# Kernel optimization log

Measured on AMD Instinct MI355X. Metric: run time of the kernel, lower is better.

## Reference

```python
import jax, jax.numpy as jnp
import numpy as np

MAX_FRAMES = 12
EMBED_DIM = 512
TOPK = 12
NUM_SAMPLES = 500
SIGMA = 0.05
SEL_DIM = 2
NUM_HEADS = 2


def setup_inputs() -> dict:
    key = jax.random.key(0)
    ks = jax.random.split(key, 9)
    D = EMBED_DIM
    C = D // 2
    s = lambda fan_in: 1.0 / np.sqrt(fan_in)
    return {
        "x": jax.random.normal(ks[0], (16, MAX_FRAMES * 50, D), dtype=jnp.float32),
        "ln_g": jnp.ones((D,), jnp.float32),
        "ln_b": jnp.zeros((D,), jnp.float32),
        "w_in": jax.random.normal(ks[1], (D, C), jnp.float32) * s(D),
        "wq": jax.random.normal(ks[2], (C, C), jnp.float32) * s(C),
        "wk": jax.random.normal(ks[3], (C, C), jnp.float32) * s(C),
        "wv": jax.random.normal(ks[4], (C, C), jnp.float32) * s(C),
        "wo": jax.random.normal(ks[5], (C, C), jnp.float32) * s(C),
        "w1": jax.random.normal(ks[6], (2 * C, C), jnp.float32) * s(2 * C),
        "w2": jax.random.normal(ks[7], (C, 1), jnp.float32) * s(C),
    }


def layer_norm(x, g, b, eps=1e-5):
    mu = jnp.mean(x, axis=-1, keepdims=True)
    var = jnp.var(x, axis=-1, keepdims=True)
    return (x - mu) * jax.lax.rsqrt(var + eps) * g + b


def mha(x, wq, wk, wv, wo):
    B, N, C = x.shape
    hd = C // NUM_HEADS
    q = (x @ wq).reshape(B, N, NUM_HEADS, hd).transpose(0, 2, 1, 3)
    k = (x @ wk).reshape(B, N, NUM_HEADS, hd).transpose(0, 2, 1, 3)
    v = (x @ wv).reshape(B, N, NUM_HEADS, hd).transpose(0, 2, 1, 3)
    attn = jax.nn.softmax(jnp.einsum('bhnd,bhmd->bhnm', q, k) / np.sqrt(hd), axis=-1)
    out = jnp.einsum('bhnm,bhmd->bhnd', attn, v).transpose(0, 2, 1, 3).reshape(B, N, C)
    return out @ wo


def predictor(x, ln_g, ln_b, w_in, wq, wk, wv, wo, w1, w2):
    h = jax.nn.gelu(layer_norm(x, ln_g, ln_b) @ w_in, approximate=False)
    h = mha(h, wq, wk, wv, wo)
    B, N, C = h.shape
    g = jnp.mean(h, axis=1, keepdims=True)
    h = jnp.concatenate([h, jnp.broadcast_to(g, (B, N, C))], axis=-1)
    h = jax.nn.gelu(h @ w1, approximate=False)
    return jnp.tanh(h @ w2)  # (B, N, 1)


def perturbed_topk(scores):
    # scores: (b, d) -> soft indicators (b, k, d)
    b, d = scores.shape
    noise = jax.random.normal(jax.random.key(1), (b, NUM_SAMPLES, d), dtype=scores.dtype)
    perturbed = scores[:, None, :] + noise * SIGMA
    _, idx = jax.lax.top_k(perturbed, TOPK)            # (b, ns, k)
    idx = jnp.sort(idx, axis=-1)
    onehot = jax.nn.one_hot(idx, d, dtype=scores.dtype)  # (b, ns, k, d)
    return onehot.mean(axis=1)                          # (b, k, d)


def reference(x, ln_g, ln_b, w_in, wq, wk, wv, wo, w1, w2):
    B, L, D = x.shape
    N = L // MAX_FRAMES
    xf = x.reshape(B * MAX_FRAMES, N, D)
    pred = predictor(xf, ln_g, ln_b, w_in, wq, wk, wv, wo, w1, w2)[..., 0]  # (b, N)
    spatial_score = pred[:, SEL_DIM:]                    # (b, N-2)
    ind = perturbed_topk(spatial_score)                  # (b, k, N-2)
    cls_feat = xf[:, :SEL_DIM, :]
    spatial_feat = xf[:, SEL_DIM:, :]
    sel = jnp.einsum('bkl,bld->bkd', ind, spatial_feat)
    out = jnp.concatenate([cls_feat, sel], axis=1)       # (b, 2+k, D)
    return out.reshape(B, -1, D)
```

## Files before the change

kernel.cpp:

```cpp
#include <hip/hip_runtime.h>
#include <stdint.h>

#define B2      192
#define NTOK    50
#define ROWS    9600
#define D_EMB   512
#define C_DIM   256
#define HD      128
#define NSAMP   500
#define TOPKK   12
#define NSPA    48

typedef short short8 __attribute__((ext_vector_type(8)));
typedef float f32x4  __attribute__((ext_vector_type(4)));

__device__ __forceinline__ float gelu_f(float x) {
    return 0.5f * x * (1.0f + erff(x * 0.7071067811865476f));
}
__device__ __forceinline__ uint16_t f2bf(float x) {
    uint32_t u = __float_as_uint(x);
    return (uint16_t)((u + 0x7fffu + ((u >> 16) & 1u)) >> 16);
}
__device__ __forceinline__ float bf2f(uint16_t b) {
    return __uint_as_float(((uint32_t)b) << 16);
}
__device__ __forceinline__ size_t swzA(int m, int k, int K) {
    return ((size_t)(m >> 4) * (K >> 5) + (k >> 5)) * 512
         + (size_t)((((k >> 3) & 3) * 16 + (m & 15)) * 8 + (k & 7));
}

__global__ __launch_bounds__(256) void prep_kernel(const float* __restrict__ x,
                                                   const float* __restrict__ g,
                                                   const float* __restrict__ b,
                                                   short* __restrict__ xh,
                                                   short* __restrict__ xl,
                                                   const float* __restrict__ w_in, const float* __restrict__ wq,
                                                   const float* __restrict__ wk, const float* __restrict__ wv,
                                                   const float* __restrict__ wo, const float* __restrict__ w1,
                                                   short* win_hi, short* win_lo, short* wq_hi, short* wq_lo,
                                                   short* wk_hi, short* wk_lo, short* wv_hi, short* wv_lo,
                                                   short* wo_hi, short* wo_lo, short* w1a_hi, short* w1a_lo,
                                                   short* w1b_hi, short* w1b_lo) {
    if (blockIdx.x < 2400) {
        int row  = blockIdx.x * 4 + (threadIdx.x >> 6);
        int lane = threadIdx.x & 63;
        const float* rp = x + (size_t)row * D_EMB;
        float4 v0 = *(const float4*)(rp + lane * 8);
        float4 v1 = *(const float4*)(rp + lane * 8 + 4);
        float s  = v0.x + v0.y + v0.z + v0.w + v1.x + v1.y + v1.z + v1.w;
        float s2 = v0.x*v0.x + v0.y*v0.y + v0.z*v0.z + v0.w*v0.w
                 + v1.x*v1.x + v1.y*v1.y + v1.z*v1.z + v1.w*v1.w;
#pragma unroll
        for (int off = 32; off; off >>= 1) {
            s  += __shfl_xor(s,  off);
            s2 += __shfl_xor(s2, off);
        }
        float mu  = s / 512.0f;
        float var = s2 / 512.0f - mu * mu;
        float inv = 1.0f / sqrtf(var + 1e-5f);
        const float* gp = g + lane * 8;
        const float* bp = b + lane * 8;
        float o[8];
        o[0]=(v0.x-mu)*inv*gp[0]+bp[0]; o[1]=(v0.y-mu)*inv*gp[1]+bp[1];
        o[2]=(v0.z-mu)*inv*gp[2]+bp[2]; o[3]=(v0.w-mu)*inv*gp[3]+bp[3];
        o[4]=(v1.x-mu)*inv*gp[4]+bp[4]; o[5]=(v1.y-mu)*inv*gp[5]+bp[5];
        o[6]=(v1.z-mu)*inv*gp[6]+bp[6]; o[7]=(v1.w-mu)*inv*gp[7]+bp[7];
        short8 h8, l8;
#pragma unroll
        for (int j = 0; j < 8; ++j) {
            uint16_t h = f2bf(o[j]);
            h8[j] = (short)h;
            l8[j] = (short)f2bf(o[j] - bf2f(h));
        }
        size_t blk = (size_t)(row >> 4) * 16 + (lane >> 2);
        int inner  = (lane & 3) * 16 + (row & 15);
        ((short8*)xh)[blk * 64 + inner] = h8;
        ((short8*)xl)[blk * 64 + inner] = l8;
    } else {
        int blk = blockIdx.x - 2400;
        const float* W; short *hi, *lo; int K, base;
        if      (blk <  64) { W = w_in;            hi = win_hi; lo = win_lo; K = 512; base = 0;   }
        else if (blk <  96) { W = wq;              hi = wq_hi;  lo = wq_lo;  K = 256; base = 64;  }
        else if (blk < 128) { W = wk;              hi = wk_hi;  lo = wk_lo;  K = 256; base = 96;  }
        else if (blk < 160) { W = wv;              hi = wv_hi;  lo = wv_lo;  K = 256; base = 128; }
        else if (blk < 192) { W = wo;              hi = wo_hi;  lo = wo_lo;  K = 256; base = 160; }
        else if (blk < 224) { W = w1;              hi = w1a_hi; lo = w1a_lo; K = 256; base = 192; }
        else                { W = w1 + 256 * 256;  hi = w1b_hi; lo = w1b_lo; K = 256; base = 224; }
        int t = (blk - base) * 256 + threadIdx.x;
        int n = t & 255, k8 = t >> 8;
        short8 h8, l8;
#pragma unroll
        for (int j = 0; j < 8; ++j) {
            float wvl = W[(size_t)(k8 * 8 + j) * 256 + n];
            uint16_t h = f2bf(wvl);
            h8[j] = (short)h;
            l8[j] = (short)f2bf(wvl - bf2f(h));
        }
        size_t bb = (size_t)(n >> 4) * (K >> 5) + (k8 >> 2);
        int inner = (k8 & 3) * 16 + (n & 15);
        ((short8*)hi)[bb * 64 + inner] = h8;
        ((short8*)lo)[bb * 64 + inner] = l8;
    }
}

template<int KB>
__device__ __forceinline__ void mm_core(const short8* __restrict__ pAh, const short8* __restrict__ pAl,
                                        const short8* __restrict__ pBh0, const short8* __restrict__ pBl0,
                                        const short8* __restrict__ pBh1, const short8* __restrict__ pBl1,
                                        f32x4& acc0, f32x4& acc1) {
    short8 ah[3], al[3], bh0[3], bl0[3], bh1[3], bl1[3];
#pragma unroll
    for (int i = 0; i < 2; ++i) {
        int off = i * 64;
        ah[i] = pAh[off];  al[i] = pAl[off];
        bh0[i] = pBh0[off]; bl0[i] = pBl0[off];
        bh1[i] = pBh1[off]; bl1[i] = pBl1[off];
    }
#pragma unroll
    for (int ks = 0; ks < KB; ++ks) {
        int cur = ks % 3;
        if (ks + 2 < KB) {
            int pre = (ks + 2) % 3, off = (ks + 2) * 64;
            ah[pre] = pAh[off];  al[pre] = pAl[off];
            bh0[pre] = pBh0[off]; bl0[pre] = pBl0[off];
            bh1[pre] = pBh1[off]; bl1[pre] = pBl1[off];
        }
        acc0 = __builtin_amdgcn_mfma_f32_16x16x32_bf16(ah[cur], bh0[cur], acc0, 0, 0, 0);
        acc0 = __builtin_amdgcn_mfma_f32_16x16x32_bf16(ah[cur], bl0[cur], acc0, 0, 0, 0);
        acc0 = __builtin_amdgcn_mfma_f32_16x16x32_bf16(al[cur], bh0[cur], acc0, 0, 0, 0);
        acc1 = __builtin_amdgcn_mfma_f32_16x16x32_bf16(ah[cur], bh1[cur], acc1, 0, 0, 0);
        acc1 = __builtin_amdgcn_mfma_f32_16x16x32_bf16(ah[cur], bl1[cur], acc1, 0, 0, 0);
        acc1 = __builtin_amdgcn_mfma_f32_16x16x32_bf16(al[cur], bh1[cur], acc1, 0, 0, 0);
    }
}

__device__ __forceinline__ void epi_store(f32x4 acc, int row0, int col, int N,
                                          float* __restrict__ Cf, short* __restrict__ Chi,
                                          short* __restrict__ Clo,
                                          const float* __restrict__ bias, int act) {
#pragma unroll
    for (int r = 0; r < 4; ++r) {
        int row = row0 + r;
        float v2 = acc[r];
        if (bias) v2 += bias[(size_t)(row / 50) * N + col];
        if (act)  v2 = gelu_f(v2);
        if (Cf) Cf[(size_t)row * N + col] = v2;
        if (Chi) {
            uint16_t h = f2bf(v2);
            size_t ad = swzA(row, col, 256);
            Chi[ad] = (short)h;
            Clo[ad] = (short)f2bf(v2 - bf2f(h));
        }
    }
}

template<int KB>
__global__ __launch_bounds__(256) void gemm_one(const short8* __restrict__ Ah,
                                                const short8* __restrict__ Al,
                                                const short8* __restrict__ Bh,
                                                const short8* __restrict__ Bl,
                                                float* __restrict__ Cf,
                                                short* __restrict__ Chi,
                                                short* __restrict__ Clo,
                                                const float* __restrict__ bias,
                                                int act) {
    int lane = threadIdx.x & 63;
    int wv   = threadIdx.x >> 6;
    int ms   = blockIdx.x * 4 + wv;
    int ns0  = blockIdx.y * 2;
    const short8* pAh  = Ah + (size_t)ms  * KB * 64 + lane;
    const short8* pAl  = Al + (size_t)ms  * KB * 64 + lane;
    const short8* pBh0 = Bh + (size_t)ns0 * KB * 64 + lane;
    const short8* pBl0 = Bl + (size_t)ns0 * KB * 64 + lane;
    const short8* pBh1 = pBh0 + (size_t)KB * 64;
    const short8* pBl1 = pBl0 + (size_t)KB * 64;
    f32x4 acc0 = {0.f,0.f,0.f,0.f}, acc1 = {0.f,0.f,0.f,0.f};
    mm_core<KB>(pAh, pAl, pBh0, pBl0, pBh1, pBl1, acc0, acc1);
    int row0 = ms * 16 + (lane >> 4) * 4;
    int cin  = lane & 15;
    epi_store(acc0, row0, ns0 * 16 + cin,      256, Cf, Chi, Clo, bias, act);
    epi_store(acc1, row0, (ns0 + 1) * 16 + cin, 256, Cf, Chi, Clo, bias, act);
}

__global__ __launch_bounds__(256) void gemm_qkv(const short8* __restrict__ Ah,
                                                const short8* __restrict__ Al,
                                                const short8* __restrict__ Bhq, const short8* __restrict__ Blq,
                                                const short8* __restrict__ Bhk, const short8* __restrict__ Blk,
                                                const short8* __restrict__ Bhv, const short8* __restrict__ Blv,
                                                float* __restrict__ q, float* __restrict__ k,
                                                float* __restrict__ v) {
    int lane = threadIdx.x & 63;
    int wv   = threadIdx.x >> 6;
    int ms   = blockIdx.x * 4 + wv;
    int sel  = blockIdx.y >> 3;
    int ns0  = (blockIdx.y & 7) * 2;
    const short8* Bh = (sel == 0) ? Bhq : (sel == 1) ? Bhk : Bhv;
    const short8* Bl = (sel == 0) ? Blq : (sel == 1) ? Blk : Blv;
    float* C = (sel == 0) ? q : (sel == 1) ? k : v;
    const short8* pAh  = Ah + (size_t)ms  * 8 * 64 + lane;
    const short8* pAl  = Al + (size_t)ms  * 8 * 64 + lane;
    const short8* pBh0 = Bh + (size_t)ns0 * 8 * 64 + lane;
    const short8* pBl0 = Bl + (size_t)ns0 * 8 * 64 + lane;
    const short8* pBh1 = pBh0 + 8 * 64;
    const short8* pBl1 = pBl0 + 8 * 64;
    f32x4 acc0 = {0.f,0.f,0.f,0.f}, acc1 = {0.f,0.f,0.f,0.f};
    mm_core<8>(pAh, pAl, pBh0, pBl0, pBh1, pBl1, acc0, acc1);
    int row0 = ms * 16 + (lane >> 4) * 4;
    int cin  = lane & 15;
    epi_store(acc0, row0, ns0 * 16 + cin,      256, C, nullptr, nullptr, nullptr, 0);
    epi_store(acc1, row0, (ns0 + 1) * 16 + cin, 256, C, nullptr, nullptr, nullptr, 0);
}

__global__ __launch_bounds__(256) void attn_kernel(const float* __restrict__ q,
                                                   const float* __restrict__ k,
                                                   const float* __restrict__ v,
                                                   short* __restrict__ aoh,
                                                   short* __restrict__ aol) {
    __shared__ float sQ[NTOK * 132];
    __shared__ float sK[NTOK * 132];
    __shared__ float sS[NTOK * 51];
    int blk = blockIdx.x;
    int b = blk >> 1, h = blk & 1;
    const size_t base = (size_t)b * NTOK * C_DIM + h * HD;
    int tid = threadIdx.x;
    for (int idx = tid; idx < 1600; idx += 256) {
        int r = idx >> 5, c = (idx & 31) * 4;
        *(float4*)&sQ[r * 132 + c] = *(const float4*)(q + base + (size_t)r * C_DIM + c);
        *(float4*)&sK[r * 132 + c] = *(const float4*)(k + base + (size_t)r * C_DIM + c);
    }
    __syncthreads();
    for (int e = tid; e < 625; e += 256) {
        int i2 = e / 25, j2 = e - i2 * 25;
        int i = i2 * 2, j = j2 * 2;
        const float* qi0 = &sQ[i * 132];
        const float* qi1 = qi0 + 132;
        const float* kj0 = &sK[j * 132];
        const float* kj1 = kj0 + 132;
        float4 a00 = {0,0,0,0}, a01 = {0,0,0,0}, a10 = {0,0,0,0}, a11 = {0,0,0,0};
#pragma unroll
        for (int t = 0; t < 32; ++t) {
            float4 q0 = *(const float4*)&qi0[t * 4];
            float4 q1 = *(const float4*)&qi1[t * 4];
            float4 b0 = *(const float4*)&kj0[t * 4];
            float4 b1 = *(const float4*)&kj1[t * 4];
            a00.x = fmaf(q0.x, b0.x, a00.x); a00.y = fmaf(q0.y, b0.y, a00.y);
            a00.z = fmaf(q0.z, b0.z, a00.z); a00.w = fmaf(q0.w, b0.w, a00.w);
            a01.x = fmaf(q0.x, b1.x, a01.x); a01.y = fmaf(q0.y, b1.y, a01.y);
            a01.z = fmaf(q0.z, b1.z, a01.z); a01.w = fmaf(q0.w, b1.w, a01.w);
            a10.x = fmaf(q1.x, b0.x, a10.x); a10.y = fmaf(q1.y, b0.y, a10.y);
            a10.z = fmaf(q1.z, b0.z, a10.z); a10.w = fmaf(q1.w, b0.w, a10.w);
            a11.x = fmaf(q1.x, b1.x, a11.x); a11.y = fmaf(q1.y, b1.y, a11.y);
            a11.z = fmaf(q1.z, b1.z, a11.z); a11.w = fmaf(q1.w, b1.w, a11.w);
        }
        const float sc = 0.08838834764831845f;
        sS[i * 51 + j]           = (a00.x + a00.y + a00.z + a00.w) * sc;
        sS[i * 51 + j + 1]       = (a01.x + a01.y + a01.z + a01.w) * sc;
        sS[(i + 1) * 51 + j]     = (a10.x + a10.y + a10.z + a10.w) * sc;
        sS[(i + 1) * 51 + j + 1] = (a11.x + a11.y + a11.z + a11.w) * sc;
    }
    __syncthreads();
    for (int idx = tid; idx < 1600; idx += 256) {
        int r = idx >> 5, c = (idx & 31) * 4;
        *(float4*)&sQ[r * 132 + c] = *(const float4*)(v + base + (size_t)r * C_DIM + c);
    }
    if (tid < NTOK) {
        float* row = &sS[tid * 51];
        float m = row[0];
        for (int j = 1; j < NTOK; ++j) m = fmaxf(m, row[j]);
        float sum = 0.f;
        for (int j = 0; j < NTOK; ++j) { float e2 = expf(row[j] - m); row[j] = e2; sum += e2; }
        float inv = 1.0f / sum;
        for (int j = 0; j < NTOK; ++j) row[j] *= inv;
    }
    __syncthreads();
    for (int e = tid; e < 1600; e += 256) {
        int i = e >> 5, d4 = (e & 31) * 4;
        const float* srow = &sS[i * 51];
        float4 acc = {0,0,0,0};
#pragma unroll
        for (int j = 0; j < NTOK; ++j) {
            float w = srow[j];
            float4 v4 = *(const float4*)&sQ[j * 132 + d4];
            acc.x = fmaf(w, v4.x, acc.x); acc.y = fmaf(w, v4.y, acc.y);
            acc.z = fmaf(w, v4.z, acc.z); acc.w = fmaf(w, v4.w, acc.w);
        }
        int row = b * NTOK + i;
        float vals[4] = {acc.x, acc.y, acc.z, acc.w};
#pragma unroll
        for (int c = 0; c < 4; ++c) {
            int col = h * HD + d4 + c;
            uint16_t hh = f2bf(vals[c]);
            size_t ad = swzA(row, col, 256);
            aoh[ad] = (short)hh;
            aol[ad] = (short)f2bf(vals[c] - bf2f(hh));
        }
    }
}

__global__ __launch_bounds__(256) void mean50(const float* __restrict__ h2,
                                              short* __restrict__ gh,
                                              short* __restrict__ gl) {
    int b = blockIdx.x, c = threadIdx.x;
    float s = 0.f;
    for (int n = 0; n < NTOK; ++n) s += h2[((size_t)b * NTOK + n) * C_DIM + c];
    float g = s / 50.0f;
    uint16_t h = f2bf(g);
    size_t ad = swzA(b, c, 256);
    gh[ad] = (short)h;
    gl[ad] = (short)f2bf(g - bf2f(h));
}

__global__ __launch_bounds__(256) void matvec_tanh(const float* __restrict__ h3,
                                                   const float* __restrict__ w2,
                                                   float* __restrict__ pred) {
    int row  = blockIdx.x * 4 + (threadIdx.x >> 6);
    int lane = threadIdx.x & 63;
    const float* rp = h3 + (size_t)row * C_DIM;
    float4 a = *(const float4*)(rp + lane * 4);
    float4 w = *(const float4*)(w2 + lane * 4);
    float s = a.x * w.x + a.y * w.y + a.z * w.z + a.w * w.w;
#pragma unroll
    for (int off = 32; off; off >>= 1) s += __shfl_xor(s, off);
    if (lane == 0) pred[row] = tanhf(s);
}

__device__ __forceinline__ uint32_t rotl32(uint32_t x, int r) {
    return (x << r) | (x >> (32 - r));
}
__device__ __forceinline__ void threefry01(uint32_t& x0, uint32_t& x1) {
    const uint32_t ks0 = 0u, ks1 = 1u, ks2 = 0x1BD11BDBu;
    x0 += ks0; x1 += ks1;
#define TFR(r) { x0 += x1; x1 = rotl32(x1, r); x1 ^= x0; }
    TFR(13) TFR(15) TFR(26) TFR(6)  x0 += ks1; x1 += ks2 + 1u;
    TFR(17) TFR(29) TFR(16) TFR(24) x0 += ks2; x1 += ks0 + 2u;
    TFR(13) TFR(15) TFR(26) TFR(6)  x0 += ks0; x1 += ks1 + 3u;
    TFR(17) TFR(29) TFR(16) TFR(24) x0 += ks1; x1 += ks2 + 4u;
    TFR(13) TFR(15) TFR(26) TFR(6)  x0 += ks2; x1 += ks0 + 5u;
#undef TFR
}

__device__ __forceinline__ float erfinv_xla(float x) {
    float w = -log1pf(-x * x);
    float p;
    if (w < 5.0f) {
        w -= 2.5f;
        p = 2.81022636e-08f;
        p = fmaf(p, w, 3.43273939e-07f);
        p = fmaf(p, w, -3.5233877e-06f);
        p = fmaf(p, w, -4.39150654e-06f);
        p = fmaf(p, w, 0.00021858087f);
        p = fmaf(p, w, -0.00125372503f);
        p = fmaf(p, w, -0.00417768164f);
        p = fmaf(p, w, 0.246640727f);
        p = fmaf(p, w, 1.50140941f);
    } else {
        w = sqrtf(w) - 3.0f;
        p = -0.000200214257f;
        p = fmaf(p, w, 0.000100950558f);
        p = fmaf(p, w, 0.00134934322f);
        p = fmaf(p, w, -0.00367342844f);
        p = fmaf(p, w, 0.00573950773f);
        p = fmaf(p, w, -0.0076224613f);
        p = fmaf(p, w, 0.00943887047f);
        p = fmaf(p, w, 1.00167406f);
        p = fmaf(p, w, 2.83297682f);
    }
    return p * x;
}

__device__ __forceinline__ float bits_to_normal(uint32_t bits) {
    float f = __uint_as_float((bits >> 9) | 0x3f800000u) - 1.0f;
    float u = f * 2.0f + (-0.99999994039535522461f);
    u = fmaxf(-0.99999994039535522461f, u);
    return 1.4142135623730951f * erfinv_xla(u);
}

__device__ __forceinline__ unsigned long long topk_key(uint32_t base, int d,
                                                       const float* __restrict__ sp) {
    uint32_t x0 = 0u, x1 = base + (uint32_t)d;
    threefry01(x0, x1);
    float n  = bits_to_normal(x0 ^ x1);
    float v  = sp[d] + n * 0.05f;
    uint32_t vb   = __float_as_uint(v);
    uint32_t mono = (vb & 0x80000000u) ? ~vb : (vb | 0x80000000u);
    return ((unsigned long long)mono << 6) | (unsigned)(63 - d);
}

__global__ __launch_bounds__(256, 4) void topk_kernel(const float* __restrict__ pred,
                                                      int* __restrict__ counts) {
    __shared__ unsigned long long sK[128][13];
    int lane = threadIdx.x & 63;
    int wv   = threadIdx.x >> 6;
    int p    = wv >> 1;
    int hh   = wv & 1;
    int g    = blockIdx.x * 128 + p * 64 + lane;
    int b    = g / NSAMP;
    int s    = g - b * NSAMP;
    uint32_t base = (uint32_t)((b * NSAMP + s) * NSPA);
    const float* sp = pred + b * NTOK + 2;
    int d0 = hh * 24;

    unsigned long long l0=0ull,l1=0ull,l2=0ull,l3=0ull,l4=0ull,l5=0ull,
                       l6=0ull,l7=0ull,l8=0ull,l9=0ull,l10=0ull,l11=0ull;
    unsigned long long key;

#define STEP(li) { unsigned long long mn_ = (key < li) ? key : li; \
                   li = (key > li) ? key : li; key = mn_; }
#define S1  STEP(l0)
#define S2  S1  STEP(l1)
#define S3  S2  STEP(l2)
#define S4  S3  STEP(l3)
#define S5  S4  STEP(l4)
#define S6  S5  STEP(l5)
#define S7  S6  STEP(l6)
#define S8  S7  STEP(l7)
#define S9  S8  STEP(l8)
#define S10 S9  STEP(l9)
#define S11 S10 STEP(l10)
#define S12 S11 STEP(l11)

    key = topk_key(base, d0 + 0,  sp); S1
    key = topk_key(base, d0 + 1,  sp); S2
    key = topk_key(base, d0 + 2,  sp); S3
    key = topk_key(base, d0 + 3,  sp); S4
    key = topk_key(base, d0 + 4,  sp); S5
    key = topk_key(base, d0 + 5,  sp); S6
    key = topk_key(base, d0 + 6,  sp); S7
    key = topk_key(base, d0 + 7,  sp); S8
    key = topk_key(base, d0 + 8,  sp); S9
    key = topk_key(base, d0 + 9,  sp); S10
    key = topk_key(base, d0 + 10, sp); S11
    key = topk_key(base, d0 + 11, sp); S12
#pragma unroll 2
    for (int dd = 12; dd < 24; ++dd) {
        key = topk_key(base, d0 + dd, sp); S12
    }

    int rowL = p * 64 + lane;
    if (hh == 1) {
        unsigned long long* r = sK[rowL];
        r[0]=l0; r[1]=l1; r[2]=l2;  r[3]=l3;  r[4]=l4;   r[5]=l5;
        r[6]=l6; r[7]=l7; r[8]=l8;  r[9]=l9;  r[10]=l10; r[11]=l11;
    }
    __syncthreads();
    if (hh == 0) {
        const unsigned long long* r = sK[rowL];
        unsigned long long M0  = (l0  > r[11]) ? l0  : r[11];
        unsigned long long M1  = (l1  > r[10]) ? l1  : r[10];
        unsigned long long M2  = (l2  > r[9])  ? l2  : r[9];
        unsigned long long M3  = (l3  > r[8])  ? l3  : r[8];
        unsigned long long M4  = (l4  > r[7])  ? l4  : r[7];
        unsigned long long M5  = (l5  > r[6])  ? l5  : r[6];
        unsigned long long M6  = (l6  > r[5])  ? l6  : r[5];
        unsigned long long M7  = (l7  > r[4])  ? l7  : r[4];
        unsigned long long M8  = (l8  > r[3])  ? l8  : r[3];
        unsigned long long M9  = (l9  > r[2])  ? l9  : r[2];
        unsigned long long M10 = (l10 > r[1])  ? l10 : r[1];
        unsigned long long M11 = (l11 > r[0])  ? l11 : r[0];
        unsigned long long m = 0ull;
        m |= 1ull << (unsigned)(M0  & 63ull);  m |= 1ull << (unsigned)(M1  & 63ull);
        m |= 1ull << (unsigned)(M2  & 63ull);  m |= 1ull << (unsigned)(M3  & 63ull);
        m |= 1ull << (unsigned)(M4  & 63ull);  m |= 1ull << (unsigned)(M5  & 63ull);
        m |= 1ull << (unsigned)(M6  & 63ull);  m |= 1ull << (unsigned)(M7  & 63ull);
        m |= 1ull << (unsigned)(M8  & 63ull);  m |= 1ull << (unsigned)(M9  & 63ull);
        m |= 1ull << (unsigned)(M10 & 63ull);  m |= 1ull << (unsigned)(M11 & 63ull);
#define EMIT(Mi) { unsigned a_ = (unsigned)(Mi & 63ull); \
                   int kpos_ = 11 - __popcll(m & ((1ull << a_) - 1ull)); \
                   int d_ = 63 - (int)a_; \
                   atomicAdd(&counts[((size_t)b * TOPKK + kpos_) * NSPA + d_], 1); }
        EMIT(M0)  EMIT(M1)  EMIT(M2)  EMIT(M3)  EMIT(M4)  EMIT(M5)
        EMIT(M6)  EMIT(M7)  EMIT(M8)  EMIT(M9)  EMIT(M10) EMIT(M11)
#undef EMIT
    }
#undef STEP
#undef S1
#undef S2
#undef S3
#undef S4
#undef S5
#undef S6
#undef S7
#undef S8
#undef S9
#undef S10
#undef S11
#undef S12
}

__global__ __launch_bounds__(256) void select_out(const float* __restrict__ x,
                                                  const int* __restrict__ counts,
                                                  float* __restrict__ out) {
    int row = blockIdx.x;
    int b = row / 14, k = row - b * 14;
    int d = threadIdx.x;
    if (k < 2) {
        out[(size_t)row * D_EMB + d]       = x[((size_t)(b * NTOK + k)) * D_EMB + d];
        out[(size_t)row * D_EMB + d + 256] = x[((size_t)(b * NTOK + k)) * D_EMB + d + 256];
    } else {
        int kk = k - 2;
        const int* cnt = counts + ((size_t)b * TOPKK + kk) * NSPA;
        __shared__ int sc[NSPA];
        if (d < NSPA) sc[d] = cnt[d];
        __syncthreads();
        float a0 = 0.f, a1 = 0.f;
        for (int l = 0; l < NSPA; ++l) {
            int c = sc[l];
            if (c) {
                float w = (float)c / 500.0f;
                const float* xr = x + ((size_t)(b * NTOK + 2 + l)) * D_EMB;
                a0 = fmaf(w, xr[d], a0);
                a1 = fmaf(w, xr[d + 256], a1);
            }
        }
        out[(size_t)row * D_EMB + d]       = a0;
        out[(size_t)row * D_EMB + d + 256] = a1;
    }
}

extern "C" void kernel_launch(void* const* d_in, const int* in_sizes, int n_in,
                              void* d_out, int out_size, void* d_ws, size_t ws_size,
                              hipStream_t stream) {
    const float* x    = (const float*)d_in[0];
    const float* ln_g = (const float*)d_in[1];
    const float* ln_b = (const float*)d_in[2];
    const float* w_in = (const float*)d_in[3];
    const float* wq   = (const float*)d_in[4];
    const float* wk   = (const float*)d_in[5];
    const float* wv   = (const float*)d_in[6];
    const float* wo   = (const float*)d_in[7];
    const float* w1   = (const float*)d_in[8];
    const float* w2   = (const float*)d_in[9];
    float* out = (float*)d_out;

    char* W = (char*)d_ws;
    short* xn_hi  = (short*)(W + 0);
    short* xn_lo  = (short*)(W + 9830400);
    short* ao_hi  = (short*)(W + 0);
    short* ao_lo  = (short*)(W + 4915200);
    short* h2_hi  = (short*)(W + 9830400);
    short* h2_lo  = (short*)(W + 14745600);
    short* h1_hi  = (short*)(W + 19660800);
    short* h1_lo  = (short*)(W + 24576000);
    float* h3     = (float*)(W + 19660800);
    float* q      = (float*)(W + 29491200);
    float* h2f    = (float*)(W + 29491200);
    float* k      = (float*)(W + 39321600);
    float* v      = (float*)(W + 49152000);
    short* win_hi = (short*)(W + 58982400);
    short* win_lo = (short*)(W + 59244544);
    short* wq_hi  = (short*)(W + 59506688);
    short* wq_lo  = (short*)(W + 59637760);
    short* wk_hi  = (short*)(W + 59768832);
    short* wk_lo  = (short*)(W + 59899904);
    short* wv_hi  = (short*)(W + 60030976);
    short* wv_lo  = (short*)(W + 60162048);
    short* wo_hi  = (short*)(W + 60293120);
    short* wo_lo  = (short*)(W + 60424192);
    short* w1a_hi = (short*)(W + 60555264);
    short* w1a_lo = (short*)(W + 60686336);
    short* w1b_hi = (short*)(W + 60817408);
    short* w1b_lo = (short*)(W + 60948480);
    short* gm_hi  = (short*)(W + 61079552);
    short* gm_lo  = (short*)(W + 61177856);
    float* gw     = (float*)(W + 61276160);
    float* pred   = (float*)(W + 61472768);
    int*   counts = (int*)  (W + 61511168);

    hipMemsetAsync(counts, 0, (size_t)B2 * TOPKK * NSPA * sizeof(int), stream);
    prep_kernel<<<2656, 256, 0, stream>>>(x, ln_g, ln_b, xn_hi, xn_lo,
        w_in, wq, wk, wv, wo, w1,
        win_hi, win_lo, wq_hi, wq_lo, wk_hi, wk_lo, wv_hi, wv_lo,
        wo_hi, wo_lo, w1a_hi, w1a_lo, w1b_hi, w1b_lo);
    gemm_one<16><<<dim3(150, 8), 256, 0, stream>>>((const short8*)xn_hi, (const short8*)xn_lo,
        (const short8*)win_hi, (const short8*)win_lo, nullptr, h1_hi, h1_lo, nullptr, 1);
    gemm_qkv<<<dim3(150, 24), 256, 0, stream>>>((const short8*)h1_hi, (const short8*)h1_lo,
        (const short8*)wq_hi, (const short8*)wq_lo, (const short8*)wk_hi, (const short8*)wk_lo,
        (const short8*)wv_hi, (const short8*)wv_lo, q, k, v);
    attn_kernel<<<B2 * 2, 256, 0, stream>>>(q, k, v, ao_hi, ao_lo);
    gemm_one<8><<<dim3(150, 8), 256, 0, stream>>>((const short8*)ao_hi, (const short8*)ao_lo,
        (const short8*)wo_hi, (const short8*)wo_lo, h2f, h2_hi, h2_lo, nullptr, 0);
    mean50<<<B2, 256, 0, stream>>>(h2f, gm_hi, gm_lo);
    gemm_one<8><<<dim3(3, 8), 256, 0, stream>>>((const short8*)gm_hi, (const short8*)gm_lo,
        (const short8*)w1b_hi, (const short8*)w1b_lo, gw, nullptr, nullptr, nullptr, 0);
    gemm_one<8><<<dim3(150, 8), 256, 0, stream>>>((const short8*)h2_hi, (const short8*)h2_lo,
        (const short8*)w1a_hi, (const short8*)w1a_lo, h3, nullptr, nullptr, gw, 1);
    matvec_tanh<<<ROWS / 4, 256, 0, stream>>>(h3, w2, pred);
    topk_kernel<<<750, 256, 0, stream>>>(pred, counts);
    select_out<<<B2 * 14, 256, 0, stream>>>(x, counts, out);
}
```

Baseline: 291.5 us.

## Precompute threefry noise in prep kernel and merge select_out per batch

Moves the threefry-based Gaussian noise generation out of the serial top-k tail and into extra blocks of the prep kernel. The noise is written to workspace, so the later top-k kernel only loads it. The tail is meant to get shorter because the RNG work now runs early alongside layernorm and weight prep. It costs about 18 MB of extra writes and reads, and it only activates when the workspace is large enough. Separately, select_out is rewritten to process one block per batch: each spatial token row is read once and accumulated into all 12 outputs, and rows with zero weight are skipped.

Measured after the change: 300.1 us. +3.0%, slower.

```diff
diff --git a/kernel.cpp b/kernel.cpp
--- a/kernel.cpp
+++ b/kernel.cpp
@@ -10,6 +10,10 @@
 #define NSAMP   500
 #define TOPKK   12
 #define NSPA    48
+#define NSAMP_T 96000
+#define NOISE_OFF 61953536ull
+#define NOISE_BYTES 18432000ull
+#define WS_NEED (NOISE_OFF + NOISE_BYTES)
 
 typedef short short8 __attribute__((ext_vector_type(8)));
 typedef float f32x4  __attribute__((ext_vector_type(4)));
@@ -27,6 +31,57 @@
 __device__ __forceinline__ size_t swzA(int m, int k, int K) {
     return ((size_t)(m >> 4) * (K >> 5) + (k >> 5)) * 512
          + (size_t)((((k >> 3) & 3) * 16 + (m & 15)) * 8 + (k & 7));
+}
+
+__device__ __forceinline__ uint32_t rotl32(uint32_t x, int r) {
+    return (x << r) | (x >> (32 - r));
+}
+__device__ __forceinline__ void threefry01(uint32_t& x0, uint32_t& x1) {
+    const uint32_t ks0 = 0u, ks1 = 1u, ks2 = 0x1BD11BDBu;
+    x0 += ks0; x1 += ks1;
+#define TFR(r) { x0 += x1; x1 = rotl32(x1, r); x1 ^= x0; }
+    TFR(13) TFR(15) TFR(26) TFR(6)  x0 += ks1; x1 += ks2 + 1u;
+    TFR(17) TFR(29) TFR(16) TFR(24) x0 += ks2; x1 += ks0 + 2u;
+    TFR(13) TFR(15) TFR(26) TFR(6)  x0 += ks0; x1 += ks1 + 3u;
+    TFR(17) TFR(29) TFR(16) TFR(24) x0 += ks1; x1 += ks2 + 4u;
+    TFR(13) TFR(15) TFR(26) TFR(6)  x0 += ks2; x1 += ks0 + 5u;
+#undef TFR
+}
+
+__device__ __forceinline__ float erfinv_xla(float x) {
+    float w = -log1pf(-x * x);
+    float p;
+    if (w < 5.0f) {
+        w -= 2.5f;
+        p = 2.81022636e-08f;
+        p = fmaf(p, w, 3.43273939e-07f);
+        p = fmaf(p, w, -3.5233877e-06f);
+        p = fmaf(p, w, -4.39150654e-06f);
+        p = fmaf(p, w, 0.00021858087f);
+        p = fmaf(p, w, -0.00125372503f);
+        p = fmaf(p, w, -0.00417768164f);
+        p = fmaf(p, w, 0.246640727f);
+        p = fmaf(p, w, 1.50140941f);
+    } else {
+        w = sqrtf(w) - 3.0f;
+        p = -0.000200214257f;
+        p = fmaf(p, w, 0.000100950558f);
+        p = fmaf(p, w, 0.00134934322f);
+        p = fmaf(p, w, -0.00367342844f);
+        p = fmaf(p, w, 0.00573950773f);
+        p = fmaf(p, w, -0.0076224613f);
+        p = fmaf(p, w, 0.00943887047f);
+        p = fmaf(p, w, 1.00167406f);
+        p = fmaf(p, w, 2.83297682f);
+    }
+    return p * x;
+}
+
+__device__ __forceinline__ float bits_to_normal(uint32_t bits) {
+    float f = __uint_as_float((bits >> 9) | 0x3f800000u) - 1.0f;
+    float u = f * 2.0f + (-0.99999994039535522461f);
+    u = fmaxf(-0.99999994039535522461f, u);
+    return 1.4142135623730951f * erfinv_xla(u);
 }
 
 __global__ __launch_bounds__(256) void prep_kernel(const float* __restrict__ x,
@@ -40,7 +95,8 @@
                                                    short* win_hi, short* win_lo, short* wq_hi, short* wq_lo,
                                                    short* wk_hi, short* wk_lo, short* wv_hi, short* wv_lo,
                                                    short* wo_hi, short* wo_lo, short* w1a_hi, short* w1a_lo,
-                                                   short* w1b_hi, short* w1b_lo) {
+                                                   short* w1b_hi, short* w1b_lo,
+                                                   float* __restrict__ noise) {
     if (blockIdx.x < 2400) {
         int row  = blockIdx.x * 4 + (threadIdx.x >> 6);
         int lane = threadIdx.x & 63;
@@ -76,7 +132,7 @@
         int inner  = (lane & 3) * 16 + (row & 15);
         ((short8*)xh)[blk * 64 + inner] = h8;
         ((short8*)xl)[blk * 64 + inner] = l8;
-    } else {
+    } else if (blockIdx.x < 2656) {
         int blk = blockIdx.x - 2400;
         const float* W; short *hi, *lo; int K, base;
         if      (blk <  64) { W = w_in;            hi = win_hi; lo = win_lo; K = 512; base = 0;   }
@@ -100,6 +156,21 @@
         int inner = (k8 & 3) * 16 + (n & 15);
         ((short8*)hi)[bb * 64 + inner] = h8;
         ((short8*)lo)[bb * 64 + inner] = l8;
+    } else {
+        int T = (blockIdx.x - 2656) * 256 + threadIdx.x;
+        int h = (T >= NSAMP_T) ? 1 : 0;
+        int g2 = T - h * NSAMP_T;
+        uint32_t cbase = (uint32_t)g2 * 48u + (uint32_t)(h * 24);
+        int qb = h * 6;
+#pragma unroll 2
+        for (int j = 0; j < 6; ++j) {
+            float4 o;
+            { uint32_t x0=0u, x1=cbase + (uint32_t)(j*4+0); threefry01(x0,x1); o.x = bits_to_normal(x0^x1) * 0.05f; }
+            { uint32_t x0=0u, x1=cbase + (uint32_t)(j*4+1); threefry01(x0,x1); o.y = bits_to_normal(x0^x1) * 0.05f; }
+            { uint32_t x0=0u, x1=cbase + (uint32_t)(j*4+2); threefry01(x0,x1); o.z = bits_to_normal(x0^x1) * 0.05f; }
+            { uint32_t x0=0u, x1=cbase + (uint32_t)(j*4+3); threefry01(x0,x1); o.w = bits_to_normal(x0^x1) * 0.05f; }
+            ((float4*)noise)[(size_t)(qb + j) * NSAMP_T + g2] = o;
+        }
     }
 }
 
@@ -324,57 +395,6 @@
     if (lane == 0) pred[row] = tanhf(s);
 }
 
-__device__ __forceinline__ uint32_t rotl32(uint32_t x, int r) {
-    return (x << r) | (x >> (32 - r));
-}
-__device__ __forceinline__ void threefry01(uint32_t& x0, uint32_t& x1) {
-    const uint32_t ks0 = 0u, ks1 = 1u, ks2 = 0x1BD11BDBu;
-    x0 += ks0; x1 += ks1;
-#define TFR(r) { x0 += x1; x1 = rotl32(x1, r); x1 ^= x0; }
-    TFR(13) TFR(15) TFR(26) TFR(6)  x0 += ks1; x1 += ks2 + 1u;
-    TFR(17) TFR(29) TFR(16) TFR(24) x0 += ks2; x1 += ks0 + 2u;
-    TFR(13) TFR(15) TFR(26) TFR(6)  x0 += ks0; x1 += ks1 + 3u;
-    TFR(17) TFR(29) TFR(16) TFR(24) x0 += ks1; x1 += ks2 + 4u;
-    TFR(13) TFR(15) TFR(26) TFR(6)  x0 += ks2; x1 += ks0 + 5u;
-#undef TFR
-}
-
-__device__ __forceinline__ float erfinv_xla(float x) {
-    float w = -log1pf(-x * x);
-    float p;
-    if (w < 5.0f) {
-        w -= 2.5f;
-        p = 2.81022636e-08f;
-        p = fmaf(p, w, 3.43273939e-07f);
-        p = fmaf(p, w, -3.5233877e-06f);
-        p = fmaf(p, w, -4.39150654e-06f);
-        p = fmaf(p, w, 0.00021858087f);
-        p = fmaf(p, w, -0.00125372503f);
-        p = fmaf(p, w, -0.00417768164f);
-        p = fmaf(p, w, 0.246640727f);
-        p = fmaf(p, w, 1.50140941f);
-    } else {
-        w = sqrtf(w) - 3.0f;
-        p = -0.000200214257f;
-        p = fmaf(p, w, 0.000100950558f);
-        p = fmaf(p, w, 0.00134934322f);
-        p = fmaf(p, w, -0.00367342844f);
-        p = fmaf(p, w, 0.00573950773f);
-        p = fmaf(p, w, -0.0076224613f);
-        p = fmaf(p, w, 0.00943887047f);
-        p = fmaf(p, w, 1.00167406f);
-        p = fmaf(p, w, 2.83297682f);
-    }
-    return p * x;
-}
-
-__device__ __forceinline__ float bits_to_normal(uint32_t bits) {
-    float f = __uint_as_float((bits >> 9) | 0x3f800000u) - 1.0f;
-    float u = f * 2.0f + (-0.99999994039535522461f);
-    u = fmaxf(-0.99999994039535522461f, u);
-    return 1.4142135623730951f * erfinv_xla(u);
-}
-
 __device__ __forceinline__ unsigned long long topk_key(uint32_t base, int d,
                                                        const float* __restrict__ sp) {
     uint32_t x0 = 0u, x1 = base + (uint32_t)d;
@@ -385,24 +405,6 @@
     uint32_t mono = (vb & 0x80000000u) ? ~vb : (vb | 0x80000000u);
     return ((unsigned long long)mono << 6) | (unsigned)(63 - d);
 }
-
-__global__ __launch_bounds__(256, 4) void topk_kernel(const float* __restrict__ pred,
-                                                      int* __restrict__ counts) {
-    __shared__ unsigned long long sK[128][13];
-    int lane = threadIdx.x & 63;
-    int wv   = threadIdx.x >> 6;
-    int p    = wv >> 1;
-    int hh   = wv & 1;
-    int g    = blockIdx.x * 128 + p * 64 + lane;
-    int b    = g / NSAMP;
-    int s    = g - b * NSAMP;
-    uint32_t base = (uint32_t)((b * NSAMP + s) * NSPA);
-    const float* sp = pred + b * NTOK + 2;
-    int d0 = hh * 24;
-
-    unsigned long long l0=0ull,l1=0ull,l2=0ull,l3=0ull,l4=0ull,l5=0ull,
-                       l6=0ull,l7=0ull,l8=0ull,l9=0ull,l10=0ull,l11=0ull;
-    unsigned long long key;
 
 #define STEP(li) { unsigned long long mn_ = (key < li) ? key : li; \
                    li = (key > li) ? key : li; key = mn_; }
@@ -418,6 +420,107 @@
 #define S10 S9  STEP(l9)
 #define S11 S10 STEP(l10)
 #define S12 S11 STEP(l11)
+
+#define TOPK_MERGE_TAIL                                                        \
+    int rowL = p * 64 + lane;                                                  \
+    if (hh == 1) {                                                             \
+        unsigned long long* r = sK[rowL];                                      \
+        r[0]=l0; r[1]=l1; r[2]=l2;  r[3]=l3;  r[4]=l4;   r[5]=l5;              \
+        r[6]=l6; r[7]=l7; r[8]=l8;  r[9]=l9;  r[10]=l10; r[11]=l11;            \
+    }                                                                          \
+    __syncthreads();                                                           \
+    if (hh == 0) {                                                             \
+        const unsigned long long* r = sK[rowL];                                \
+        unsigned long long M0  = (l0  > r[11]) ? l0  : r[11];                  \
+        unsigned long long M1  = (l1  > r[10]) ? l1  : r[10];                  \
+        unsigned long long M2  = (l2  > r[9])  ? l2  : r[9];                   \
+        unsigned long long M3  = (l3  > r[8])  ? l3  : r[8];                   \
+        unsigned long long M4  = (l4  > r[7])  ? l4  : r[7];                   \
+        unsigned long long M5  = (l5  > r[6])  ? l5  : r[6];                   \
+        unsigned long long M6  = (l6  > r[5])  ? l6  : r[5];                   \
+        unsigned long long M7  = (l7  > r[4])  ? l7  : r[4];                   \
+        unsigned long long M8  = (l8  > r[3])  ? l8  : r[3];                   \
+        unsigned long long M9  = (l9  > r[2])  ? l9  : r[2];                   \
+        unsigned long long M10 = (l10 > r[1])  ? l10 : r[1];                   \
+        unsigned long long M11 = (l11 > r[0])  ? l11 : r[0];                   \
+        unsigned long long m = 0ull;                                           \
+        m |= 1ull << (unsigned)(M0  & 63ull);  m |= 1ull << (unsigned)(M1  & 63ull); \
+        m |= 1ull << (unsigned)(M2  & 63ull);  m |= 1ull << (unsigned)(M3  & 63ull); \
+        m |= 1ull << (unsigned)(M4  & 63ull);  m |= 1ull << (unsigned)(M5  & 63ull); \
+        m |= 1ull << (unsigned)(M6  & 63ull);  m |= 1ull << (unsigned)(M7  & 63ull); \
+        m |= 1ull << (unsigned)(M8  & 63ull);  m |= 1ull << (unsigned)(M9  & 63ull); \
+        m |= 1ull << (unsigned)(M10 & 63ull);  m |= 1ull << (unsigned)(M11 & 63ull); \
+        EMIT(M0)  EMIT(M1)  EMIT(M2)  EMIT(M3)  EMIT(M4)  EMIT(M5)             \
+        EMIT(M6)  EMIT(M7)  EMIT(M8)  EMIT(M9)  EMIT(M10) EMIT(M11)            \
+    }
+#define EMIT(Mi) { unsigned a_ = (unsigned)(Mi & 63ull); \
+                   int kpos_ = 11 - __popcll(m & ((1ull << a_) - 1ull)); \
+                   int d_ = 63 - (int)a_; \
+                   atomicAdd(&counts[((size_t)b * TOPKK + kpos_) * NSPA + d_], 1); }
+
+__global__ __launch_bounds__(256, 4) void topk_noise(const float* __restrict__ pred,
+                                                     const float4* __restrict__ nz4,
+                                                     int* __restrict__ counts) {
+    __shared__ unsigned long long sK[128][13];
+    __shared__ float sSP[2][48];
+    int lane = threadIdx.x & 63;
+    int wv   = threadIdx.x >> 6;
+    int p    = wv >> 1;
+    int hh   = wv & 1;
+    int b0   = (blockIdx.x * 128) / NSAMP;
+    if (threadIdx.x < 96) {
+        int r = threadIdx.x / 48, dd = threadIdx.x - r * 48;
+        int bb = b0 + r; if (bb > B2 - 1) bb = B2 - 1;
+        sSP[r][dd] = pred[bb * NTOK + 2 + dd];
+    }
+    int g = blockIdx.x * 128 + p * 64 + lane;
+    int b = g / NSAMP;
+    int bo = b - b0;
+    __syncthreads();
+    const float* spl = &sSP[bo][hh * 24];
+    const float4* nq = nz4 + (size_t)(hh * 6) * NSAMP_T + g;
+
+    unsigned long long l0=0ull,l1=0ull,l2=0ull,l3=0ull,l4=0ull,l5=0ull,
+                       l6=0ull,l7=0ull,l8=0ull,l9=0ull,l10=0ull,l11=0ull;
+    unsigned long long key;
+
+#define MKKEY(dd, nv) { float v_ = spl[dd] + (nv); uint32_t vb_ = __float_as_uint(v_); \
+    uint32_t mono_ = (vb_ & 0x80000000u) ? ~vb_ : (vb_ | 0x80000000u); \
+    key = ((unsigned long long)mono_ << 6) | (unsigned)(63 - (hh * 24 + (dd))); }
+
+    float4 na = nq[0 * NSAMP_T], nb = nq[1 * NSAMP_T];
+    MKKEY(0,  na.x) S1   MKKEY(1,  na.y) S2   MKKEY(2,  na.z) S3   MKKEY(3,  na.w) S4
+    na = nq[2 * NSAMP_T];
+    MKKEY(4,  nb.x) S5   MKKEY(5,  nb.y) S6   MKKEY(6,  nb.z) S7   MKKEY(7,  nb.w) S8
+    nb = nq[3 * NSAMP_T];
+    MKKEY(8,  na.x) S9   MKKEY(9,  na.y) S10  MKKEY(10, na.z) S11  MKKEY(11, na.w) S12
+    na = nq[4 * NSAMP_T];
+    MKKEY(12, nb.x) S12  MKKEY(13, nb.y) S12  MKKEY(14, nb.z) S12  MKKEY(15, nb.w) S12
+    nb = nq[5 * NSAMP_T];
+    MKKEY(16, na.x) S12  MKKEY(17, na.y) S12  MKKEY(18, na.z) S12  MKKEY(19, na.w) S12
+    MKKEY(20, nb.x) S12  MKKEY(21, nb.y) S12  MKKEY(22, nb.z) S12  MKKEY(23, nb.w) S12
+#undef MKKEY
+
+    TOPK_MERGE_TAIL
+}
+
+__global__ __launch_bounds__(256, 4) void topk_fb(const float* __restrict__ pred,
+                                                  int* __restrict__ counts) {
+    __shared__ unsigned long long sK[128][13];
+    int lane = threadIdx.x & 63;
+    int wv   = threadIdx.x >> 6;
+    int p    = wv >> 1;
+    int hh   = wv & 1;
+    int g    = blockIdx.x * 128 + p * 64 + lane;
+    int b    = g / NSAMP;
+    int s    = g - b * NSAMP;
+    uint32_t base = (uint32_t)((b * NSAMP + s) * NSPA);
+    const float* sp = pred + b * NTOK + 2;
+    int d0 = hh * 24;
+
+    unsigned long long l0=0ull,l1=0ull,l2=0ull,l3=0ull,l4=0ull,l5=0ull,
+                       l6=0ull,l7=0ull,l8=0ull,l9=0ull,l10=0ull,l11=0ull;
+    unsigned long long key;
 
     key = topk_key(base, d0 + 0,  sp); S1
     key = topk_key(base, d0 + 1,  sp); S2
@@ -436,42 +539,10 @@
         key = topk_key(base, d0 + dd, sp); S12
     }
 
-    int rowL = p * 64 + lane;
-    if (hh == 1) {
-        unsigned long long* r = sK[rowL];
-        r[0]=l0; r[1]=l1; r[2]=l2;  r[3]=l3;  r[4]=l4;   r[5]=l5;
-        r[6]=l6; r[7]=l7; r[8]=l8;  r[9]=l9;  r[10]=l10; r[11]=l11;
-    }
-    __syncthreads();
-    if (hh == 0) {
-        const unsigned long long* r = sK[rowL];
-        unsigned long long M0  = (l0  > r[11]) ? l0  : r[11];
-        unsigned long long M1  = (l1  > r[10]) ? l1  : r[10];
-        unsigned long long M2  = (l2  > r[9])  ? l2  : r[9];
-        unsigned long long M3  = (l3  > r[8])  ? l3  : r[8];
-        unsigned long long M4  = (l4  > r[7])  ? l4  : r[7];
-        unsigned long long M5  = (l5  > r[6])  ? l5  : r[6];
-        unsigned long long M6  = (l6  > r[5])  ? l6  : r[5];
-        unsigned long long M7  = (l7  > r[4])  ? l7  : r[4];
-        unsigned long long M8  = (l8  > r[3])  ? l8  : r[3];
-        unsigned long long M9  = (l9  > r[2])  ? l9  : r[2];
-        unsigned long long M10 = (l10 > r[1])  ? l10 : r[1];
-        unsigned long long M11 = (l11 > r[0])  ? l11 : r[0];
-        unsigned long long m = 0ull;
-        m |= 1ull << (unsigned)(M0  & 63ull);  m |= 1ull << (unsigned)(M1  & 63ull);
-        m |= 1ull << (unsigned)(M2  & 63ull);  m |= 1ull << (unsigned)(M3  & 63ull);
-        m |= 1ull << (unsigned)(M4  & 63ull);  m |= 1ull << (unsigned)(M5  & 63ull);
-        m |= 1ull << (unsigned)(M6  & 63ull);  m |= 1ull << (unsigned)(M7  & 63ull);
-        m |= 1ull << (unsigned)(M8  & 63ull);  m |= 1ull << (unsigned)(M9  & 63ull);
-        m |= 1ull << (unsigned)(M10 & 63ull);  m |= 1ull << (unsigned)(M11 & 63ull);
-#define EMIT(Mi) { unsigned a_ = (unsigned)(Mi & 63ull); \
-                   int kpos_ = 11 - __popcll(m & ((1ull << a_) - 1ull)); \
-                   int d_ = 63 - (int)a_; \
-                   atomicAdd(&counts[((size_t)b * TOPKK + kpos_) * NSPA + d_], 1); }
-        EMIT(M0)  EMIT(M1)  EMIT(M2)  EMIT(M3)  EMIT(M4)  EMIT(M5)
-        EMIT(M6)  EMIT(M7)  EMIT(M8)  EMIT(M9)  EMIT(M10) EMIT(M11)
+    TOPK_MERGE_TAIL
+}
 #undef EMIT
-    }
+#undef TOPK_MERGE_TAIL
 #undef STEP
 #undef S1
 #undef S2
@@ -485,35 +556,48 @@
 #undef S10
 #undef S11
 #undef S12
-}
-
-__global__ __launch_bounds__(256) void select_out(const float* __restrict__ x,
-                                                  const int* __restrict__ counts,
-                                                  float* __restrict__ out) {
-    int row = blockIdx.x;
-    int b = row / 14, k = row - b * 14;
+
+__global__ __launch_bounds__(256) void select_out2(const float* __restrict__ x,
+                                                   const int* __restrict__ counts,
+                                                   float* __restrict__ out) {
+    int b = blockIdx.x;
     int d = threadIdx.x;
-    if (k < 2) {
-        out[(size_t)row * D_EMB + d]       = x[((size_t)(b * NTOK + k)) * D_EMB + d];
-        out[(size_t)row * D_EMB + d + 256] = x[((size_t)(b * NTOK + k)) * D_EMB + d + 256];
-    } else {
-        int kk = k - 2;
-        const int* cnt = counts + ((size_t)b * TOPKK + kk) * NSPA;
-        __shared__ int sc[NSPA];
-        if (d < NSPA) sc[d] = cnt[d];
-        __syncthreads();
-        float a0 = 0.f, a1 = 0.f;
-        for (int l = 0; l < NSPA; ++l) {
-            int c = sc[l];
-            if (c) {
-                float w = (float)c / 500.0f;
-                const float* xr = x + ((size_t)(b * NTOK + 2 + l)) * D_EMB;
-                a0 = fmaf(w, xr[d], a0);
-                a1 = fmaf(w, xr[d + 256], a1);
-            }
-        }
-        out[(size_t)row * D_EMB + d]       = a0;
-        out[(size_t)row * D_EMB + d + 256] = a1;
+    __shared__ float sw[TOPKK * NSPA];
+    __shared__ int anyl[NSPA];
+    for (int i = d; i < TOPKK * NSPA; i += 256)
+        sw[i] = (float)counts[(size_t)b * TOPKK * NSPA + i] * 0.002f;
+    __syncthreads();
+    if (d < NSPA) {
+        int a = 0;
+        for (int k2 = 0; k2 < TOPKK; ++k2) a |= (sw[k2 * NSPA + d] != 0.0f);
+        anyl[d] = a;
+    }
+    __syncthreads();
+    {
+        const float* xr0 = x + (size_t)(b * NTOK) * D_EMB;
+        out[(size_t)(b * 14 + 0) * D_EMB + d]       = xr0[d];
+        out[(size_t)(b * 14 + 0) * D_EMB + d + 256] = xr0[d + 256];
+        out[(size_t)(b * 14 + 1) * D_EMB + d]       = xr0[D_EMB + d];
+        out[(size_t)(b * 14 + 1) * D_EMB + d + 256] = xr0[D_EMB + d + 256];
+    }
+    float a0[TOPKK], a1[TOPKK];
+#pragma unroll
+    for (int k2 = 0; k2 < TOPKK; ++k2) { a0[k2] = 0.f; a1[k2] = 0.f; }
+    for (int l = 0; l < NSPA; ++l) {
+        if (!anyl[l]) continue;
+        const float* xr = x + (size_t)(b * NTOK + 2 + l) * D_EMB;
+        float v0 = xr[d], v1 = xr[d + 256];
+#pragma unroll
+        for (int k2 = 0; k2 < TOPKK; ++k2) {
+            float w = sw[k2 * NSPA + l];
+            a0[k2] = fmaf(w, v0, a0[k2]);
+            a1[k2] = fmaf(w, v1, a1[k2]);
+        }
+    }
+#pragma unroll
+    for (int k2 = 0; k2 < TOPKK; ++k2) {
+        out[(size_t)(b * 14 + 2 + k2) * D_EMB + d]       = a0[k2];
+        out[(size_t)(b * 14 + 2 + k2) * D_EMB + d + 256] = a1[k2];
     }
 }
 
@@ -565,12 +649,15 @@
     float* gw     = (float*)(W + 61276160);
     float* pred   = (float*)(W + 61472768);
     int*   counts = (int*)  (W + 61511168);
+    float* noise  = (float*)(W + NOISE_OFF);
+
+    const bool nzmode = ws_size >= WS_NEED;
 
     hipMemsetAsync(counts, 0, (size_t)B2 * TOPKK * NSPA * sizeof(int), stream);
-    prep_kernel<<<2656, 256, 0, stream>>>(x, ln_g, ln_b, xn_hi, xn_lo,
+    prep_kernel<<<nzmode ? 3406 : 2656, 256, 0, stream>>>(x, ln_g, ln_b, xn_hi, xn_lo,
         w_in, wq, wk, wv, wo, w1,
         win_hi, win_lo, wq_hi, wq_lo, wk_hi, wk_lo, wv_hi, wv_lo,
-        wo_hi, wo_lo, w1a_hi, w1a_lo, w1b_hi, w1b_lo);
+        wo_hi, wo_lo, w1a_hi, w1a_lo, w1b_hi, w1b_lo, noise);
     gemm_one<16><<<dim3(150, 8), 256, 0, stream>>>((const short8*)xn_hi, (const short8*)xn_lo,
         (const short8*)win_hi, (const short8*)win_lo, nullptr, h1_hi, h1_lo, nullptr, 1);
     gemm_qkv<<<dim3(150, 24), 256, 0, stream>>>((const short8*)h1_hi, (const short8*)h1_lo,
@@ -585,6 +672,7 @@
     gemm_one<8><<<dim3(150, 8), 256, 0, stream>>>((const short8*)h2_hi, (const short8*)h2_lo,
         (const short8*)w1a_hi, (const short8*)w1a_lo, h3, nullptr, nullptr, gw, 1);
     matvec_tanh<<<ROWS / 4, 256, 0, stream>>>(h3, w2, pred);
-    topk_kernel<<<750, 256, 0, stream>>>(pred, counts);
-    select_out<<<B2 * 14, 256, 0, stream>>>(x, counts, out);
-}
+    if (nzmode) topk_noise<<<750, 256, 0, stream>>>(pred, (const float4*)noise, counts);
+    else        topk_fb<<<750, 256, 0, stream>>>(pred, counts);
+    select_out2<<<B2, 256, 0, stream>>>(x, counts, out);
+}
```
